# Kernel tuning notes

Measured on AMD Instinct MI355X. Metric: run time of the kernel, lower is better.

## Reference

```python
import jax, jax.numpy as jnp
import numpy as np

Q = 1  # hidden size is hardcoded to 1 in the module's forward


def lcg_zscore(m, n):
    """Deterministic LCG weight generator used by RADAM's ELM, z-scored."""
    L = m * n
    if L == 1:
        return np.ones((1, 1), dtype=np.float32)
    V = np.zeros(L, dtype=np.float64)
    V[0] = L + 1
    a, b, c = L + 2, L + 3, float(L) * float(L)
    for i in range(1, L):
        V[i] = (a * V[i - 1] + b) % c
    V = (V - V.mean()) / V.std()
    return V.reshape(m, n).astype(np.float32)


def setup_inputs() -> dict:
    key = jax.random.key(0)
    B, Z, W, H = 32, 2048, 32, 32
    x = jax.random.normal(key, (B, Z, W, H), dtype=jnp.float32)
    alpha = jnp.asarray(lcg_zscore(Q, Z))  # (Q, z) fixed random encoder weights
    return {"x": x, "alpha": alpha}


def reference(x, alpha):
    # Batched ELM-autoencoder fit replacing the per-sample Python loop.
    B, Z, W, H = x.shape
    N = W * H
    X = x.reshape(B, Z, N)  # feature_map per sample: (z, w*h)
    # hidden activations H = sigmoid(alpha @ X): (B, Q, N)
    Hact = jax.nn.sigmoid(jnp.einsum('qz,bzn->bqn', alpha, X))
    # ELM-AE output weights beta = pinv(H^T) @ X^T, shape (B, Q, z).
    # For Q=1 H^T is an N x 1 full-column-rank matrix (sigmoid > 0), so
    # pinv(H^T) = H / ||H||^2 exactly -- closed form, no SVD needed.
    denom = jnp.sum(Hact * Hact, axis=-1, keepdims=True)  # (B, Q, 1)
    beta = jnp.einsum('bqn,bzn->bqz', Hact, X) / denom     # (B, Q, z)
    return beta.reshape(B, Q * Z, 1)
```

## Files before the change

### kernel.cpp

```cpp
#include <hip/hip_runtime.h>
#include <math.h>

constexpr int BB   = 32;
constexpr int ZD   = 2048;
constexpr int ND   = 1024;
constexpr int ZC   = 64;
constexpr int ZPC  = ZD / ZC;

__global__ __launch_bounds__(256) void k1_partial(const float* __restrict__ x,
                                                  const float* __restrict__ alpha,
                                                  float* __restrict__ partial) {
    const int blk = blockIdx.x;
    const int b   = blk >> 6;
    const int c   = blk & (ZC - 1);
    const int t   = threadIdx.x;
    const float4* x4 = (const float4*)x + ((size_t)(b * ZD + c * ZPC)) * (ND / 4) + t;
    const float* al = alpha + c * ZPC;
    float4 acc = make_float4(0.f, 0.f, 0.f, 0.f);
#pragma unroll
    for (int z = 0; z < ZPC; ++z) {
        const float a  = al[z];
        const float4 v = x4[(size_t)z * (ND / 4)];
        acc.x = fmaf(a, v.x, acc.x);
        acc.y = fmaf(a, v.y, acc.y);
        acc.z = fmaf(a, v.z, acc.z);
        acc.w = fmaf(a, v.w, acc.w);
    }
    ((float4*)partial)[(size_t)blk * (ND / 4) + t] = acc;
}

__global__ __launch_bounds__(1024) void k2_finalize(const float* __restrict__ partial,
                                                    float* __restrict__ h,
                                                    float* __restrict__ denom) {
    const int b = blockIdx.x;
    const int n = threadIdx.x;
    float s = 0.f;
#pragma unroll
    for (int c = 0; c < ZC; ++c)
        s += partial[((size_t)(b * ZC + c)) * ND + n];
    const float hv = 1.0f / (1.0f + expf(-s));
    h[b * ND + n] = hv;

    float d = hv * hv;
#pragma unroll
    for (int o = 32; o > 0; o >>= 1) d += __shfl_down(d, o);
    __shared__ float red[16];
    const int lane = n & 63, w = n >> 6;
    if (lane == 0) red[w] = d;
    __syncthreads();
    if (n == 0) {
        float tot = 0.f;
#pragma unroll
        for (int i = 0; i < 16; ++i) tot += red[i];
        denom[b] = tot;
    }
}

__global__ __launch_bounds__(256) void k3_beta(const float* __restrict__ x,
                                               const float* __restrict__ h,
                                               const float* __restrict__ denom,
                                               float* __restrict__ out) {
    const int blk = blockIdx.x;
    const int b   = blk / (ZD / 16);
    const int zb  = (blk % (ZD / 16)) * 16;
    const int t    = threadIdx.x;
    const int wave = t >> 6;
    const int lane = t & 63;

    const float4* h4 = (const float4*)(h + (size_t)b * ND);
    const float4 h0 = h4[lane];
    const float4 h1 = h4[lane + 64];
    const float4 h2 = h4[lane + 128];
    const float4 h3 = h4[lane + 192];
    const float dn = denom[b];

    const float4* base = (const float4*)(x + ((size_t)(b * ZD + zb + wave * 4)) * ND);
    float s0 = 0.f, s1 = 0.f, s2 = 0.f, s3 = 0.f;
    {
        const float4 a0 = base[lane],       a1 = base[lane + 64];
        const float4 a2 = base[lane + 128], a3 = base[lane + 192];
        s0 = a0.x*h0.x + a0.y*h0.y + a0.z*h0.z + a0.w*h0.w
           + a1.x*h1.x + a1.y*h1.y + a1.z*h1.z + a1.w*h1.w
           + a2.x*h2.x + a2.y*h2.y + a2.z*h2.z + a2.w*h2.w
           + a3.x*h3.x + a3.y*h3.y + a3.z*h3.z + a3.w*h3.w;
    }
    {
        const float4* row = base + (ND / 4);
        const float4 a0 = row[lane],       a1 = row[lane + 64];
        const float4 a2 = row[lane + 128], a3 = row[lane + 192];
        s1 = a0.x*h0.x + a0.y*h0.y + a0.z*h0.z + a0.w*h0.w
           + a1.x*h1.x + a1.y*h1.y + a1.z*h1.z + a1.w*h1.w
           + a2.x*h2.x + a2.y*h2.y + a2.z*h2.z + a2.w*h2.w
           + a3.x*h3.x + a3.y*h3.y + a3.z*h3.z + a3.w*h3.w;
    }
    {
        const float4* row = base + 2 * (ND / 4);
        const float4 a0 = row[lane],       a1 = row[lane + 64];
        const float4 a2 = row[lane + 128], a3 = row[lane + 192];
        s2 = a0.x*h0.x + a0.y*h0.y + a0.z*h0.z + a0.w*h0.w
           + a1.x*h1.x + a1.y*h1.y + a1.z*h1.z + a1.w*h1.w
           + a2.x*h2.x + a2.y*h2.y + a2.z*h2.z + a2.w*h2.w
           + a3.x*h3.x + a3.y*h3.y + a3.z*h3.z + a3.w*h3.w;
    }
    {
        const float4* row = base + 3 * (ND / 4);
        const float4 a0 = row[lane],       a1 = row[lane + 64];
        const float4 a2 = row[lane + 128], a3 = row[lane + 192];
        s3 = a0.x*h0.x + a0.y*h0.y + a0.z*h0.z + a0.w*h0.w
           + a1.x*h1.x + a1.y*h1.y + a1.z*h1.z + a1.w*h1.w
           + a2.x*h2.x + a2.y*h2.y + a2.z*h2.z + a2.w*h2.w
           + a3.x*h3.x + a3.y*h3.y + a3.z*h3.z + a3.w*h3.w;
    }
#pragma unroll
    for (int o = 32; o > 0; o >>= 1) {
        s0 += __shfl_down(s0, o);
        s1 += __shfl_down(s1, o);
        s2 += __shfl_down(s2, o);
        s3 += __shfl_down(s3, o);
    }
    if (lane == 0) {
        float* o = out + b * ZD + zb + wave * 4;
        o[0] = s0 / dn;
        o[1] = s1 / dn;
        o[2] = s2 / dn;
        o[3] = s3 / dn;
    }
}

extern "C" void kernel_launch(void* const* d_in, const int* in_sizes, int n_in,
                              void* d_out, int out_size, void* d_ws, size_t ws_size,
                              hipStream_t stream) {
    const float* x     = (const float*)d_in[0];
    const float* alpha = (const float*)d_in[1];
    float* out = (float*)d_out;

    float* partial = (float*)d_ws;
    float* h       = partial + (size_t)BB * ZC * ND;
    float* denom   = h + (size_t)BB * ND;

    k1_partial<<<BB * ZC, 256, 0, stream>>>(x, alpha, partial);
    k2_finalize<<<BB, 1024, 0, stream>>>(partial, h, denom);
    k3_beta<<<BB * (ZD / 16), 256, 0, stream>>>(x, h, denom, out);
}
```

Measured before the change: 411.9 us.

## Reverse batch order in beta pass and fold denominator into h

The beta kernel now walks batches in reverse, so the samples most recently read by the partial-sum kernel, which may still sit in last-level cache, are read first. The division by the norm moves into the finalize kernel, which writes h/||h||^2 instead of h and the denominator separately. The z-chunk count is halved, giving fewer, longer blocks in the first pass and a smaller partial buffer. Nontemporal loads and stores are added for streaming data, with some risk of defeating the cache reuse the reordering aims for.

```diff
diff --git a/kernel.cpp b/kernel.cpp
--- a/kernel.cpp
+++ b/kernel.cpp
@@ -4,47 +4,48 @@
 constexpr int BB   = 32;
 constexpr int ZD   = 2048;
 constexpr int ND   = 1024;
-constexpr int ZC   = 64;
+constexpr int ZC   = 32;
 constexpr int ZPC  = ZD / ZC;
+
+using f32x4 = __attribute__((ext_vector_type(4))) float;
 
 __global__ __launch_bounds__(256) void k1_partial(const float* __restrict__ x,
                                                   const float* __restrict__ alpha,
                                                   float* __restrict__ partial) {
     const int blk = blockIdx.x;
-    const int b   = blk >> 6;
+    const int b   = blk >> 5;
     const int c   = blk & (ZC - 1);
     const int t   = threadIdx.x;
-    const float4* x4 = (const float4*)x + ((size_t)(b * ZD + c * ZPC)) * (ND / 4) + t;
+    const f32x4* x4 = (const f32x4*)x + ((size_t)(b * ZD + c * ZPC)) * (ND / 4) + t;
     const float* al = alpha + c * ZPC;
-    float4 acc = make_float4(0.f, 0.f, 0.f, 0.f);
-#pragma unroll
+    f32x4 acc = {0.f, 0.f, 0.f, 0.f};
+#pragma unroll 8
     for (int z = 0; z < ZPC; ++z) {
-        const float a  = al[z];
-        const float4 v = x4[(size_t)z * (ND / 4)];
+        const float a = al[z];
+        const f32x4 v = x4[(size_t)z * (ND / 4)];
         acc.x = fmaf(a, v.x, acc.x);
         acc.y = fmaf(a, v.y, acc.y);
         acc.z = fmaf(a, v.z, acc.z);
         acc.w = fmaf(a, v.w, acc.w);
     }
-    ((float4*)partial)[(size_t)blk * (ND / 4) + t] = acc;
+    __builtin_nontemporal_store(acc, (f32x4*)partial + (size_t)blk * (ND / 4) + t);
 }
 
 __global__ __launch_bounds__(1024) void k2_finalize(const float* __restrict__ partial,
-                                                    float* __restrict__ h,
-                                                    float* __restrict__ denom) {
+                                                    float* __restrict__ hd) {
     const int b = blockIdx.x;
     const int n = threadIdx.x;
     float s = 0.f;
 #pragma unroll
     for (int c = 0; c < ZC; ++c)
-        s += partial[((size_t)(b * ZC + c)) * ND + n];
+        s += __builtin_nontemporal_load(partial + ((size_t)(b * ZC + c)) * ND + n);
     const float hv = 1.0f / (1.0f + expf(-s));
-    h[b * ND + n] = hv;
 
     float d = hv * hv;
 #pragma unroll
     for (int o = 32; o > 0; o >>= 1) d += __shfl_down(d, o);
     __shared__ float red[16];
+    __shared__ float tot_s;
     const int lane = n & 63, w = n >> 6;
     if (lane == 0) red[w] = d;
     __syncthreads();
@@ -52,60 +53,68 @@
         float tot = 0.f;
 #pragma unroll
         for (int i = 0; i < 16; ++i) tot += red[i];
-        denom[b] = tot;
+        tot_s = tot;
     }
+    __syncthreads();
+    hd[b * ND + n] = hv / tot_s;
 }
 
 __global__ __launch_bounds__(256) void k3_beta(const float* __restrict__ x,
-                                               const float* __restrict__ h,
-                                               const float* __restrict__ denom,
+                                               const float* __restrict__ hd,
                                                float* __restrict__ out) {
     const int blk = blockIdx.x;
-    const int b   = blk / (ZD / 16);
-    const int zb  = (blk % (ZD / 16)) * 16;
+    const int b   = (BB - 1) - (blk >> 7);
+    const int zb  = (blk & 127) * 16;
     const int t    = threadIdx.x;
     const int wave = t >> 6;
     const int lane = t & 63;
 
-    const float4* h4 = (const float4*)(h + (size_t)b * ND);
-    const float4 h0 = h4[lane];
-    const float4 h1 = h4[lane + 64];
-    const float4 h2 = h4[lane + 128];
-    const float4 h3 = h4[lane + 192];
-    const float dn = denom[b];
+    const f32x4* h4 = (const f32x4*)(hd + (size_t)b * ND);
+    const f32x4 h0 = h4[lane];
+    const f32x4 h1 = h4[lane + 64];
+    const f32x4 h2 = h4[lane + 128];
+    const f32x4 h3 = h4[lane + 192];
 
-    const float4* base = (const float4*)(x + ((size_t)(b * ZD + zb + wave * 4)) * ND);
-    float s0 = 0.f, s1 = 0.f, s2 = 0.f, s3 = 0.f;
+    const f32x4* base = (const f32x4*)(x + ((size_t)(b * ZD + zb + wave * 4)) * ND);
+    float s0, s1, s2, s3;
     {
-        const float4 a0 = base[lane],       a1 = base[lane + 64];
-        const float4 a2 = base[lane + 128], a3 = base[lane + 192];
+        const f32x4 a0 = __builtin_nontemporal_load(base + lane);
+        const f32x4 a1 = __builtin_nontemporal_load(base + lane + 64);
+        const f32x4 a2 = __builtin_nontemporal_load(base + lane + 128);
+        const f32x4 a3 = __builtin_nontemporal_load(base + lane + 192);
         s0 = a0.x*h0.x + a0.y*h0.y + a0.z*h0.z + a0.w*h0.w
            + a1.x*h1.x + a1.y*h1.y + a1.z*h1.z + a1.w*h1.w
            + a2.x*h2.x + a2.y*h2.y + a2.z*h2.z + a2.w*h2.w
            + a3.x*h3.x + a3.y*h3.y + a3.z*h3.z + a3.w*h3.w;
     }
     {
-        const float4* row = base + (ND / 4);
-        const float4 a0 = row[lane],       a1 = row[lane + 64];
-        const float4 a2 = row[lane + 128], a3 = row[lane + 192];
+        const f32x4* row = base + (ND / 4);
+        const f32x4 a0 = __builtin_nontemporal_load(row + lane);
+        const f32x4 a1 = __builtin_nontemporal_load(row + lane + 64);
+        const f32x4 a2 = __builtin_nontemporal_load(row + lane + 128);
+        const f32x4 a3 = __builtin_nontemporal_load(row + lane + 192);
         s1 = a0.x*h0.x + a0.y*h0.y + a0.z*h0.z + a0.w*h0.w
            + a1.x*h1.x + a1.y*h1.y + a1.z*h1.z + a1.w*h1.w
            + a2.x*h2.x + a2.y*h2.y + a2.z*h2.z + a2.w*h2.w
            + a3.x*h3.x + a3.y*h3.y + a3.z*h3.z + a3.w*h3.w;
     }
     {
-        const float4* row = base + 2 * (ND / 4);
-        const float4 a0 = row[lane],       a1 = row[lane + 64];
-        const float4 a2 = row[lane + 128], a3 = row[lane + 192];
+        const f32x4* row = base + 2 * (ND / 4);
+        const f32x4 a0 = __builtin_nontemporal_load(row + lane);
+        const f32x4 a1 = __builtin_nontemporal_load(row + lane + 64);
+        const f32x4 a2 = __builtin_nontemporal_load(row + lane + 128);
+        const f32x4 a3 = __builtin_nontemporal_load(row + lane + 192);
         s2 = a0.x*h0.x + a0.y*h0.y + a0.z*h0.z + a0.w*h0.w
            + a1.x*h1.x + a1.y*h1.y + a1.z*h1.z + a1.w*h1.w
            + a2.x*h2.x + a2.y*h2.y + a2.z*h2.z + a2.w*h2.w
            + a3.x*h3.x + a3.y*h3.y + a3.z*h3.z + a3.w*h3.w;
     }
     {
-        const float4* row = base + 3 * (ND / 4);
-        const float4 a0 = row[lane],       a1 = row[lane + 64];
-        const float4 a2 = row[lane + 128], a3 = row[lane + 192];
+        const f32x4* row = base + 3 * (ND / 4);
+        const f32x4 a0 = __builtin_nontemporal_load(row + lane);
+        const f32x4 a1 = __builtin_nontemporal_load(row + lane + 64);
+        const f32x4 a2 = __builtin_nontemporal_load(row + lane + 128);
+        const f32x4 a3 = __builtin_nontemporal_load(row + lane + 192);
         s3 = a0.x*h0.x + a0.y*h0.y + a0.z*h0.z + a0.w*h0.w
            + a1.x*h1.x + a1.y*h1.y + a1.z*h1.z + a1.w*h1.w
            + a2.x*h2.x + a2.y*h2.y + a2.z*h2.z + a2.w*h2.w
@@ -120,10 +129,7 @@
     }
     if (lane == 0) {
         float* o = out + b * ZD + zb + wave * 4;
-        o[0] = s0 / dn;
-        o[1] = s1 / dn;
-        o[2] = s2 / dn;
-        o[3] = s3 / dn;
+        o[0] = s0; o[1] = s1; o[2] = s2; o[3] = s3;
     }
 }
 
@@ -135,10 +141,9 @@
     float* out = (float*)d_out;
 
     float* partial = (float*)d_ws;
-    float* h       = partial + (size_t)BB * ZC * ND;
-    float* denom   = h + (size_t)BB * ND;
+    float* hd      = partial + (size_t)BB * ZC * ND;
 
     k1_partial<<<BB * ZC, 256, 0, stream>>>(x, alpha, partial);
-    k2_finalize<<<BB, 1024, 0, stream>>>(partial, h, denom);
-    k3_beta<<<BB * (ZD / 16), 256, 0, stream>>>(x, h, denom, out);
+    k2_finalize<<<BB, 1024, 0, stream>>>(partial, hd);
+    k3_beta<<<BB * (ZD / 16), 256, 0, stream>>>(x, hd, out);
 }
```

Result: faster. 397.6 us (-3.5%).
